# Kernel optimization log

Measured on AMD Instinct MI355X. Metric: run time of the kernel, lower is better.

## Reference

```python
import jax, jax.numpy as jnp
import numpy as np

EPS = 1e-5

def _conv(x, w, b, pad):
    # PyTorch-style cross-correlation, NCHW / OIHW
    y = jax.lax.conv_general_dilated(
        x, w, window_strides=(1, 1),
        padding=[(pad, pad), (pad, pad)],
        dimension_numbers=('NCHW', 'OIHW', 'NCHW'))
    return y + b[None, :, None, None]

def _bn(x, gamma, beta):
    # training-mode BatchNorm2d (biased variance), as nn.BatchNorm2d defaults
    mu = x.mean(axis=(0, 2, 3), keepdims=True)
    var = ((x - mu) ** 2).mean(axis=(0, 2, 3), keepdims=True)
    xn = (x - mu) * jax.lax.rsqrt(var + EPS)
    return xn * gamma[None, :, None, None] + beta[None, :, None, None]

def _meanpool2(x):
    B, C, H, W = x.shape
    return x.reshape(B, C, H // 2, 2, W // 2, 2).mean(axis=(3, 5))

def setup_inputs() -> dict:
    key = jax.random.key(0)
    ks = jax.random.split(key, 16)
    B = 131072
    inp = {}
    inp['x'] = jax.random.normal(ks[0], (B, 1, 8, 8), dtype=jnp.float32)
    # ConvolutionLayer1: 6 independent ConvolutionN(k=3, cin=1); w scale (cin*k)**-0.5
    inp['w1'] = jax.random.normal(ks[1], (6, 1, 3, 3), dtype=jnp.float32) * (1 * 3) ** (-0.5)
    inp['b1'] = jax.random.normal(ks[2], (6,), dtype=jnp.float32) * (1 * 3) ** (-0.5)
    inp['g1'] = jnp.ones((6,), jnp.float32)
    inp['be1'] = jnp.zeros((6,), jnp.float32)
    # ConvolutionLayer2: 16 ConvolutionN(k=2, cin=6)
    inp['w2'] = jax.random.normal(ks[3], (16, 6, 2, 2), dtype=jnp.float32) * (6 * 2) ** (-0.5)
    inp['b2'] = jax.random.normal(ks[4], (16,), dtype=jnp.float32) * (6 * 2) ** (-0.5)
    inp['g2'] = jnp.ones((16,), jnp.float32)
    inp['be2'] = jnp.zeros((16,), jnp.float32)
    # FC layers (torch Linear: y = x @ W.T + b), kaiming-uniform-ish init
    def lin(k, out_d, in_d):
        k1, k2 = jax.random.split(k)
        bound = 1.0 / np.sqrt(in_d)
        W = jax.random.uniform(k1, (out_d, in_d), jnp.float32, -bound, bound)
        b = jax.random.uniform(k2, (out_d,), jnp.float32, -bound, bound)
        return W, b
    inp['fw1'], inp['fb1'] = lin(ks[5], 30, 64)
    inp['fw2'], inp['fb2'] = lin(ks[6], 15, 30)
    inp['fw3'], inp['fb3'] = lin(ks[7], 10, 15)
    return inp

def reference(x, w1, b1, g1, be1, w2, b2, g2, be2, fw1, fb1, fw2, fb2, fw3, fb3):
    h = _conv(x, w1, b1, pad=2)          # [B,6,10,10]
    h = jax.nn.relu(_bn(h, g1, be1))
    h = _meanpool2(h)                    # [B,6,5,5]
    h = _conv(h, w2, b2, pad=0)          # [B,16,4,4]
    h = jax.nn.relu(_bn(h, g2, be2))
    h = _meanpool2(h)                    # [B,16,2,2]
    h = h.reshape(h.shape[0], -1)        # [B,64]
    h = jax.nn.relu(h @ fw1.T + fb1)     # dropout = identity in eval
    h = jax.nn.relu(h @ fw2.T + fb2)
    return h @ fw3.T + fb3               # [B,10]
```

## Files before the change

kernel.cpp:

```cpp
#include <hip/hip_runtime.h>

#define WS_SUM2 0
#define WS_SQ2  16
#define WS_W1S  64
#define WS_B1S  118
#define WS_T    124
#define WS_A    125
#define WS_W2S  144
#define WS_B2S  528
#define WS_ZERO_N 144

#define PST 148
#define POOL_CST 30
#define POOL_IST 184

#define XL_F   (16 * PST)
#define POOL_F (16 * POOL_IST)

#define FW1_ST 68
#define FW1_F  (30 * FW1_ST)
#define FW2_F  (30 * 16)
#define FW3_F  (15 * 16)

#define WSYNC() asm volatile("s_waitcnt lgkmcnt(0)" ::: "memory")

__device__ __forceinline__ float wave_sum(float v) {
#pragma unroll
  for (int off = 32; off > 0; off >>= 1) v += __shfl_down(v, off, 64);
  return v;
}

__device__ __forceinline__ void zero_own_xl(float* xl) {
  const int tid = threadIdx.x;
  const int wv = tid >> 6, lane = tid & 63;
  float* wxl = xl + wv * (4 * PST);
  for (int i = lane; i < 4 * PST; i += 64) wxl[i] = 0.f;
}

__device__ __forceinline__ void write_interior(float* xl, float4 v) {
  const int tid = threadIdx.x;
  const int imgl = tid >> 4;
  const int f = (tid & 15) * 4;
  const int row = f >> 3, col = f & 7;
  float* dst = xl + imgl * PST + (row + 2) * 12 + (col + 2);
  dst[0] = v.x; dst[1] = v.y; dst[2] = v.z; dst[3] = v.w;
}

__device__ __forceinline__ void pooled_front_coop(const float* xl, float* pool,
                                                  const float* __restrict__ wsf) {
  const int tid = threadIdx.x;
  const int imgl = tid >> 4, l16 = tid & 15;
  const float* ibase = xl + imgl * PST;
  float* pbase = pool + imgl * POOL_IST;

#pragma unroll
  for (int k2 = 0; k2 < 2; ++k2) {
    const int p = l16 + 16 * k2;
    if (p < 25) {
      const int r = p / 5, s = p % 5;
      const float* wb = ibase + (2 * r) * 12 + 2 * s;
      float X[16];
#pragma unroll
      for (int a = 0; a < 4; ++a) {
        const float2* wr = reinterpret_cast<const float2*>(wb + a * 12);
        const float2 e0 = wr[0], e1 = wr[1];
        X[a * 4 + 0] = e0.x; X[a * 4 + 1] = e0.y;
        X[a * 4 + 2] = e1.x; X[a * 4 + 3] = e1.y;
      }
#pragma unroll
      for (int i = 0; i < 16; ++i) asm volatile("" : "+v"(X[i]));
#pragma unroll
      for (int c = 0; c < 6; ++c) {
        const float bc = wsf[WS_B1S + c];
        float acc = 0.f;
#pragma unroll
        for (int di = 0; di < 2; ++di) {
#pragma unroll
          for (int dj = 0; dj < 2; ++dj) {
            float z = bc;
#pragma unroll
            for (int u = 0; u < 3; ++u)
#pragma unroll
              for (int v = 0; v < 3; ++v)
                z = fmaf(wsf[WS_W1S + c * 9 + u * 3 + v],
                         X[(di + u) * 4 + dj + v], z);
            acc += fmaxf(z, 0.f);
          }
        }
        pbase[c * POOL_CST + r * 6 + s] = acc;
      }
    }
  }
}

__device__ __forceinline__ void load6(const float* p, float r[6]) {
  const float2* q = reinterpret_cast<const float2*>(p);
  const float2 a = q[0], b = q[1], c = q[2];
  r[0] = a.x; r[1] = a.y; r[2] = b.x; r[3] = b.y; r[4] = c.x; r[5] = c.y;
}

__device__ __forceinline__ void conv2_lane_lds(const float* pool,
                                               const float* w2L,
                                               const float* b2L,
                                               float yp[16]) {
  const int tid = threadIdx.x;
  const int imgl = tid >> 4, o = tid & 15;
  const float* pbase = pool + imgl * POOL_IST;

  const float yb = b2L[o];
#pragma unroll
  for (int p = 0; p < 16; ++p) yp[p] = yb;

#pragma unroll
  for (int c = 0; c < 6; ++c) {
    const float4 wv = *reinterpret_cast<const float4*>(w2L + o * 24 + c * 4);
    const float* pcb = pbase + c * POOL_CST;
    const float w00 = wv.x, w01 = wv.y, w10 = wv.z, w11 = wv.w;
    float r[2][6];
    load6(pcb, r[0]);
#pragma unroll
    for (int i2 = 0; i2 < 4; ++i2) {
      float* top = r[i2 & 1];
      float* bot = r[(i2 + 1) & 1];
      load6(pcb + (i2 + 1) * 6, bot);
#pragma unroll
      for (int j2 = 0; j2 < 4; ++j2) {
        float acc = yp[i2 * 4 + j2];
        acc = fmaf(w00, top[j2], acc);
        acc = fmaf(w01, top[j2 + 1], acc);
        acc = fmaf(w10, bot[j2], acc);
        acc = fmaf(w11, bot[j2 + 1], acc);
        yp[i2 * 4 + j2] = acc;
      }
    }
  }
}

__global__ __launch_bounds__(256) void k_stats1(
    const float* __restrict__ x, float* ws, int nblk) {
  __shared__ __align__(16) float xl[XL_F];
  __shared__ float red[4][16];
  const int tid = threadIdx.x;
  zero_own_xl(xl);

  float T = 0.f, A[13];
#pragma unroll
  for (int i = 0; i < 13; ++i) A[i] = 0.f;

  int blk = blockIdx.x;
  float4 pfx;
  if (blk < nblk)
    pfx = reinterpret_cast<const float4*>(x)[(size_t)blk * 256 + tid];
  for (; blk < nblk; blk += gridDim.x) {
    WSYNC();
    write_interior(xl, pfx);
    const int bn = blk + gridDim.x;
    if (bn < nblk)
      pfx = reinterpret_cast<const float4*>(x)[(size_t)bn * 256 + tid];
    WSYNC();
    const float* ib = xl + (tid >> 4) * PST;
    const int l16 = tid & 15;
#pragma unroll
    for (int k = 0; k < 4; ++k) {
      const int p = l16 + k * 16;
      const int r = p >> 3, c = p & 7;
      const float* q = ib + (r + 2) * 12 + (c + 2);
      const float xc = q[0];
      T += xc;
      A[0]  = fmaf(xc, q[0],  A[0]);
      A[1]  = fmaf(xc, q[1],  A[1]);
      A[2]  = fmaf(xc, q[2],  A[2]);
      A[3]  = fmaf(xc, q[10], A[3]);
      A[4]  = fmaf(xc, q[11], A[4]);
      A[5]  = fmaf(xc, q[12], A[5]);
      A[6]  = fmaf(xc, q[13], A[6]);
      A[7]  = fmaf(xc, q[14], A[7]);
      A[8]  = fmaf(xc, q[22], A[8]);
      A[9]  = fmaf(xc, q[23], A[9]);
      A[10] = fmaf(xc, q[24], A[10]);
      A[11] = fmaf(xc, q[25], A[11]);
      A[12] = fmaf(xc, q[26], A[12]);
    }
  }

  const int wid = tid >> 6, lane = tid & 63;
#pragma unroll
  for (int i = 0; i < 14; ++i) {
    const float v = wave_sum(i == 0 ? T : A[i - 1]);
    if (lane == 0) red[wid][i] = v;
  }
  __syncthreads();
  if (tid < 14) {
    const float tot = red[0][tid] + red[1][tid] + red[2][tid] + red[3][tid];
    atomicAdd(&ws[WS_T + tid], tot);
  }
}

__global__ void k_fold1(const float* __restrict__ g1,
                        const float* __restrict__ be1,
                        const float* __restrict__ w1,
                        const float* __restrict__ b1, float* ws, float NP) {
  const int c = threadIdx.x;
  if (c >= 6) return;
  float Av[13];
#pragma unroll
  for (int i = 0; i < 13; ++i) Av[i] = ws[WS_A + i];
  const float T = ws[WS_T];
  float w[9];
#pragma unroll
  for (int k = 0; k < 9; ++k) w[k] = w1[c * 9 + k];
  float sw = 0.f;
#pragma unroll
  for (int k = 0; k < 9; ++k) sw += w[k];
  float q2 = 0.f;
#pragma unroll
  for (int k1 = 0; k1 < 9; ++k1) {
    const int u1 = k1 / 3, v1 = k1 % 3;
#pragma unroll
    for (int k2 = 0; k2 < 9; ++k2) {
      int du = k2 / 3 - u1, dv = k2 % 3 - v1;
      if (du < 0 || (du == 0 && dv < 0)) { du = -du; dv = -dv; }
      const float a = (du == 0) ? Av[dv] : Av[3 + (du - 1) * 5 + dv + 2];
      q2 = fmaf(w[k1] * w[k2], a, q2);
    }
  }
  const float b = b1[c];
  const float sum1 = sw * T + NP * b;
  const float sumsq1 = q2 + 2.f * b * sw * T + NP * b * b;
  const float mean = sum1 / NP;
  const float var = sumsq1 / NP - mean * mean;
  const float sc = g1[c] * rsqrtf(var + 1e-5f);
  const float sh = be1[c] - mean * sc;
#pragma unroll
  for (int k = 0; k < 9; ++k)
    ws[WS_W1S + c * 9 + k] = w[k] * sc * 0.25f;
  ws[WS_B1S + c] = fmaf(b, sc, sh) * 0.25f;
}

__global__ void k_fold2(const float* __restrict__ g2,
                        const float* __restrict__ be2,
                        const float* __restrict__ w2,
                        const float* __restrict__ b2, float* ws, float inv_n) {
  __shared__ float scs[16];
  const int t = threadIdx.x;
  if (t < 16) {
    const float mean = ws[WS_SUM2 + t] * inv_n;
    const float var  = ws[WS_SQ2 + t] * inv_n - mean * mean;
    const float sc   = g2[t] * rsqrtf(var + 1e-5f);
    const float sh   = be2[t] - mean * sc;
    scs[t] = sc;
    ws[WS_B2S + t] = fmaf(b2[t], sc, sh);
  }
  __syncthreads();
  if (t < 384) ws[WS_W2S + t] = w2[t] * scs[t / 24];
}

__global__ __launch_bounds__(256, 4) void k_stats2(
    const float* __restrict__ x, const float* __restrict__ w2,
    const float* __restrict__ b2, float* ws, int nblk) {
  __shared__ __align__(16) float xl[XL_F];
  __shared__ __align__(16) float pool[POOL_F];
  __shared__ __align__(16) float w2L[384];
  __shared__ float b2L[16];
  __shared__ float red[4][32];
  const int tid = threadIdx.x;
  for (int d = tid; d < 384; d += 256) w2L[d] = w2[d];
  if (tid < 16) b2L[tid] = b2[tid];
  zero_own_xl(xl);
  __syncthreads();

  float s = 0.f, q = 0.f;

  int t = blockIdx.x;
  float4 pfx;
  if (t < nblk)
    pfx = reinterpret_cast<const float4*>(x)[(size_t)t * 256 + tid];
  for (; t < nblk; t += gridDim.x) {
    WSYNC();
    write_interior(xl, pfx);
    const int tn = t + gridDim.x;
    if (tn < nblk)
      pfx = reinterpret_cast<const float4*>(x)[(size_t)tn * 256 + tid];
    WSYNC();
    pooled_front_coop(xl, pool, ws);
    WSYNC();
    float yp[16];
    conv2_lane_lds(pool, w2L, b2L, yp);
#pragma unroll
    for (int p = 0; p < 16; ++p) { s += yp[p]; q = fmaf(yp[p], yp[p], q); }
  }

  s += __shfl_xor(s, 16, 64); s += __shfl_xor(s, 32, 64);
  q += __shfl_xor(q, 16, 64); q += __shfl_xor(q, 32, 64);
  const int wid = tid >> 6, lane = tid & 63;
  if (lane < 16) { red[wid][lane] = s; red[wid][16 + lane] = q; }
  __syncthreads();
  if (tid < 32) {
    const float tot = red[0][tid] + red[1][tid] + red[2][tid] + red[3][tid];
    atomicAdd(&ws[tid < 16 ? WS_SUM2 + tid : WS_SQ2 + tid - 16], tot);
  }
}

__global__ __launch_bounds__(256, 4) void k_final(
    const float* __restrict__ x, const float* __restrict__ fw1,
    const float* __restrict__ fb1, const float* __restrict__ fw2,
    const float* __restrict__ fb2, const float* __restrict__ fw3,
    const float* __restrict__ fb3, const float* __restrict__ ws,
    float* __restrict__ out, int nblk) {
  __shared__ __align__(16) float xl[XL_F];
  __shared__ __align__(16) float pool[POOL_F];
  __shared__ __align__(16) float fw1L[FW1_F];
  __shared__ __align__(16) float w2L[384];
  __shared__ float b2L[16];
  __shared__ float fb1L[32];
  __shared__ float fw2T[FW2_F];
  __shared__ float fw3T[FW3_F];
  __shared__ float fb2L[16];
  __shared__ float fb3L[16];

  const int tid = threadIdx.x;
  for (int d = tid; d < 1920; d += 256) {
    const int a = d >> 6, k = d & 63;
    fw1L[a * FW1_ST + k] = fw1[d];
  }
  for (int d = tid; d < 384; d += 256) w2L[d] = ws[WS_W2S + d];
  if (tid < 16) b2L[tid] = ws[WS_B2S + tid];
  if (tid < 32) fb1L[tid] = (tid < 30) ? fb1[tid] : 0.f;
  for (int d = tid; d < FW2_F; d += 256) {
    const int j = d >> 4, a = d & 15;
    fw2T[d] = (a < 15) ? fw2[a * 30 + j] : 0.f;
  }
  for (int d = tid; d < FW3_F; d += 256) {
    const int j = d >> 4, a = d & 15;
    fw3T[d] = (a < 10) ? fw3[a * 15 + j] : 0.f;
  }
  if (tid < 16) fb2L[tid] = (tid < 15) ? fb2[tid] : 0.f;
  if (tid < 16) fb3L[tid] = (tid < 10) ? fb3[tid] : 0.f;
  zero_own_xl(xl);
  __syncthreads();

  const int imgl = tid >> 4, al = tid & 15;
  const bool has2 = (al + 16) < 30;
  const float* ra = fw1L + al * FW1_ST;
  const float* rb = fw1L + (has2 ? (al + 16) * FW1_ST : 0);

  int t = blockIdx.x;
  float4 pfx;
  if (t < nblk)
    pfx = reinterpret_cast<const float4*>(x)[(size_t)t * 256 + tid];
  for (; t < nblk; t += gridDim.x) {
    WSYNC();
    write_interior(xl, pfx);
    const int tn = t + gridDim.x;
    if (tn < nblk)
      pfx = reinterpret_cast<const float4*>(x)[(size_t)tn * 256 + tid];
    WSYNC();
    pooled_front_coop(xl, pool, ws);
    WSYNC();
    float zp[16];
    conv2_lane_lds(pool, w2L, b2L, zp);

    float* ib = pool + imgl * POOL_IST;

    float hq[4] = {0.f, 0.f, 0.f, 0.f};
#pragma unroll
    for (int i2 = 0; i2 < 4; ++i2)
#pragma unroll
      for (int j2 = 0; j2 < 4; ++j2)
        hq[(i2 >> 1) * 2 + (j2 >> 1)] += fmaxf(zp[i2 * 4 + j2], 0.f);
    float4 hv4;
    hv4.x = 0.25f * hq[0]; hv4.y = 0.25f * hq[1];
    hv4.z = 0.25f * hq[2]; hv4.w = 0.25f * hq[3];
    *reinterpret_cast<float4*>(ib + al * 4) = hv4;
    WSYNC();

    float acc0 = fb1L[al];
    float acc1 = has2 ? fb1L[al + 16] : 0.f;
#pragma unroll
    for (int kk = 0; kk < 16; ++kk) {
      const float4 hv = *reinterpret_cast<const float4*>(ib + kk * 4);
      const float4 wa = *reinterpret_cast<const float4*>(ra + kk * 4);
      const float4 wb = *reinterpret_cast<const float4*>(rb + kk * 4);
      acc0 = fmaf(wa.x, hv.x, acc0); acc0 = fmaf(wa.y, hv.y, acc0);
      acc0 = fmaf(wa.z, hv.z, acc0); acc0 = fmaf(wa.w, hv.w, acc0);
      acc1 = fmaf(wb.x, hv.x, acc1); acc1 = fmaf(wb.y, hv.y, acc1);
      acc1 = fmaf(wb.z, hv.z, acc1); acc1 = fmaf(wb.w, hv.w, acc1);
    }
    ib[68 + al] = fmaxf(acc0, 0.f);
    if (has2) ib[68 + al + 16] = fmaxf(acc1, 0.f);
    WSYNC();

    if (al < 15) {
      float acc = fb2L[al];
#pragma unroll
      for (int j = 0; j < 30; ++j)
        acc = fmaf(fw2T[j * 16 + al], ib[68 + j], acc);
      ib[101 + al] = fmaxf(acc, 0.f);
    }
    WSYNC();

    if (al < 10) {
      float acc = fb3L[al];
#pragma unroll
      for (int j = 0; j < 15; ++j)
        acc = fmaf(fw3T[j * 16 + al], ib[101 + j], acc);
      out[(size_t)(t * 16 + imgl) * 10 + al] = acc;
    }
  }
}

extern "C" void kernel_launch(void* const* d_in, const int* in_sizes, int n_in,
                              void* d_out, int out_size, void* d_ws, size_t ws_size,
                              hipStream_t stream) {
  (void)n_in; (void)out_size; (void)ws_size;
  const float* x   = (const float*)d_in[0];
  const float* w1  = (const float*)d_in[1];
  const float* b1  = (const float*)d_in[2];
  const float* g1  = (const float*)d_in[3];
  const float* be1 = (const float*)d_in[4];
  const float* w2  = (const float*)d_in[5];
  const float* b2  = (const float*)d_in[6];
  const float* g2  = (const float*)d_in[7];
  const float* be2 = (const float*)d_in[8];
  const float* fw1 = (const float*)d_in[9];
  const float* fb1 = (const float*)d_in[10];
  const float* fw2 = (const float*)d_in[11];
  const float* fb2 = (const float*)d_in[12];
  const float* fw3 = (const float*)d_in[13];
  const float* fb3 = (const float*)d_in[14];
  float* out = (float*)d_out;
  float* ws  = (float*)d_ws;

  const int Btot = in_sizes[0] / 64;
  const int nblk = Btot / 16;
  const float NP1 = (float)Btot * 100.0f;
  const float inv_n2 = 1.0f / ((float)Btot * 16.0f);
  const int grid = nblk < 1024 ? nblk : 1024;
  const int kf_grid = nblk < 1280 ? nblk : 1280;

  hipMemsetAsync(ws, 0, WS_ZERO_N * sizeof(float), stream);

  k_stats1<<<grid, 256, 0, stream>>>(x, ws, nblk);
  k_fold1<<<1, 64, 0, stream>>>(g1, be1, w1, b1, ws, NP1);
  k_stats2<<<grid, 256, 0, stream>>>(x, w2, b2, ws, nblk);
  k_fold2<<<1, 512, 0, stream>>>(g2, be2, w2, b2, ws, inv_n2);
  k_final<<<kf_grid, 256, 0, stream>>>(x, fw1, fb1, fw2, fb2, fw3, fb3, ws,
                                       out, nblk);
}
```

Before: 156.7 us.

## Shrink LDS footprint, raise occupancy bounds and grow stats grids

Tightens the LDS strides for the staged-input and pool buffers. In the final kernel, the FC2/FC3 weights and biases move out of LDS and are read through global/scalar loads and registers. Launch bounds rise to 6 and 5 blocks per CU, and the two statistics kernels get larger grids. The goal is more resident waves and less LDS setup per block. The risks are register pressure under the tighter bounds, bank conflicts from the new strides, and uncoalesced global reads of fw2/fw3 inside the loop.

```diff
diff --git a/kernel.cpp b/kernel.cpp
--- a/kernel.cpp
+++ b/kernel.cpp
@@ -10,17 +10,15 @@
 #define WS_B2S  528
 #define WS_ZERO_N 144
 
-#define PST 148
+#define PST 146
 #define POOL_CST 30
-#define POOL_IST 184
+#define POOL_IST 180
 
 #define XL_F   (16 * PST)
 #define POOL_F (16 * POOL_IST)
 
 #define FW1_ST 68
 #define FW1_F  (30 * FW1_ST)
-#define FW2_F  (30 * 16)
-#define FW3_F  (15 * 16)
 
 #define WSYNC() asm volatile("s_waitcnt lgkmcnt(0)" ::: "memory")
 
@@ -255,7 +253,7 @@
   if (t < 384) ws[WS_W2S + t] = w2[t] * scs[t / 24];
 }
 
-__global__ __launch_bounds__(256, 4) void k_stats2(
+__global__ __launch_bounds__(256, 6) void k_stats2(
     const float* __restrict__ x, const float* __restrict__ w2,
     const float* __restrict__ b2, float* ws, int nblk) {
   __shared__ __align__(16) float xl[XL_F];
@@ -301,7 +299,7 @@
   }
 }
 
-__global__ __launch_bounds__(256, 4) void k_final(
+__global__ __launch_bounds__(256, 5) void k_final(
     const float* __restrict__ x, const float* __restrict__ fw1,
     const float* __restrict__ fb1, const float* __restrict__ fw2,
     const float* __restrict__ fb2, const float* __restrict__ fw3,
@@ -312,11 +310,6 @@
   __shared__ __align__(16) float fw1L[FW1_F];
   __shared__ __align__(16) float w2L[384];
   __shared__ float b2L[16];
-  __shared__ float fb1L[32];
-  __shared__ float fw2T[FW2_F];
-  __shared__ float fw3T[FW3_F];
-  __shared__ float fb2L[16];
-  __shared__ float fb3L[16];
 
   const int tid = threadIdx.x;
   for (int d = tid; d < 1920; d += 256) {
@@ -325,17 +318,6 @@
   }
   for (int d = tid; d < 384; d += 256) w2L[d] = ws[WS_W2S + d];
   if (tid < 16) b2L[tid] = ws[WS_B2S + tid];
-  if (tid < 32) fb1L[tid] = (tid < 30) ? fb1[tid] : 0.f;
-  for (int d = tid; d < FW2_F; d += 256) {
-    const int j = d >> 4, a = d & 15;
-    fw2T[d] = (a < 15) ? fw2[a * 30 + j] : 0.f;
-  }
-  for (int d = tid; d < FW3_F; d += 256) {
-    const int j = d >> 4, a = d & 15;
-    fw3T[d] = (a < 10) ? fw3[a * 15 + j] : 0.f;
-  }
-  if (tid < 16) fb2L[tid] = (tid < 15) ? fb2[tid] : 0.f;
-  if (tid < 16) fb3L[tid] = (tid < 10) ? fb3[tid] : 0.f;
   zero_own_xl(xl);
   __syncthreads();
 
@@ -343,6 +325,10 @@
   const bool has2 = (al + 16) < 30;
   const float* ra = fw1L + al * FW1_ST;
   const float* rb = fw1L + (has2 ? (al + 16) * FW1_ST : 0);
+  const float fb1a = fb1[al];
+  const float fb1b = has2 ? fb1[al + 16] : 0.f;
+  const float fb2a = (al < 15) ? fb2[al] : 0.f;
+  const float fb3a = (al < 10) ? fb3[al] : 0.f;
 
   int t = blockIdx.x;
   float4 pfx;
@@ -374,8 +360,8 @@
     *reinterpret_cast<float4*>(ib + al * 4) = hv4;
     WSYNC();
 
-    float acc0 = fb1L[al];
-    float acc1 = has2 ? fb1L[al + 16] : 0.f;
+    float acc0 = fb1a;
+    float acc1 = fb1b;
 #pragma unroll
     for (int kk = 0; kk < 16; ++kk) {
       const float4 hv = *reinterpret_cast<const float4*>(ib + kk * 4);
@@ -391,19 +377,19 @@
     WSYNC();
 
     if (al < 15) {
-      float acc = fb2L[al];
+      float acc = fb2a;
 #pragma unroll
       for (int j = 0; j < 30; ++j)
-        acc = fmaf(fw2T[j * 16 + al], ib[68 + j], acc);
+        acc = fmaf(fw2[al * 30 + j], ib[68 + j], acc);
       ib[101 + al] = fmaxf(acc, 0.f);
     }
     WSYNC();
 
     if (al < 10) {
-      float acc = fb3L[al];
+      float acc = fb3a;
 #pragma unroll
       for (int j = 0; j < 15; ++j)
-        acc = fmaf(fw3T[j * 16 + al], ib[101 + j], acc);
+        acc = fmaf(fw3[al * 15 + j], ib[101 + j], acc);
       out[(size_t)(t * 16 + imgl) * 10 + al] = acc;
     }
   }
@@ -435,14 +421,15 @@
   const int nblk = Btot / 16;
   const float NP1 = (float)Btot * 100.0f;
   const float inv_n2 = 1.0f / ((float)Btot * 16.0f);
-  const int grid = nblk < 1024 ? nblk : 1024;
+  const int g1rid = nblk < 2048 ? nblk : 2048;
+  const int g2rid = nblk < 1536 ? nblk : 1536;
   const int kf_grid = nblk < 1280 ? nblk : 1280;
 
   hipMemsetAsync(ws, 0, WS_ZERO_N * sizeof(float), stream);
 
-  k_stats1<<<grid, 256, 0, stream>>>(x, ws, nblk);
+  k_stats1<<<g1rid, 256, 0, stream>>>(x, ws, nblk);
   k_fold1<<<1, 64, 0, stream>>>(g1, be1, w1, b1, ws, NP1);
-  k_stats2<<<grid, 256, 0, stream>>>(x, w2, b2, ws, nblk);
+  k_stats2<<<g2rid, 256, 0, stream>>>(x, w2, b2, ws, nblk);
   k_fold2<<<1, 512, 0, stream>>>(g2, be2, w2, b2, ws, inv_n2);
   k_final<<<kf_grid, 256, 0, stream>>>(x, fw1, fb1, fw2, fb2, fw3, fb3, ws,
                                        out, nblk);
```

Result: slower. 165.7 us (+5.7%).
